# Kernel optimization log

Hardware: AMD Instinct MI355X
Metric: run time of the kernel (lower is better)

Reference implementation:

```python
import jax, jax.numpy as jnp
import numpy as np

B, S, N, C = 128, 512, 64, 1
F = N * C          # flattened feature dim = input_size * n_nodes
H = 512            # hidden_size


def _gru_imputer(x2d, m2d, Wih, Whh, bih, bhh, Wro, bro):
    """Unidirectional 1-step-ahead GRU imputer.
    x2d: [B,S,F] float, m2d: [B,S,F] bool.
    Returns (x_hat [B,S,F], h [B,S,H])."""
    dt = x2d.dtype
    h0 = jnp.zeros((x2d.shape[0], H), dtype=dt)
    xhat0 = h0 @ Wro.T + bro  # readout of initial state (== bro)

    def step(carry, inp):
        h, xhat = carry
        x_t, m_t = inp  # [B,F] float, [B,F] bool
        x_p = jnp.where(m_t, x_t, xhat)
        x_in = jnp.concatenate([x_p, m_t.astype(dt)], axis=-1)  # [B,2F]
        gi = x_in @ Wih.T + bih  # [B,3H]
        gh = h @ Whh.T + bhh     # [B,3H]
        ir, iz, inn = jnp.split(gi, 3, axis=-1)
        hr, hz, hn = jnp.split(gh, 3, axis=-1)
        r = jax.nn.sigmoid(ir + hr)
        z = jax.nn.sigmoid(iz + hz)
        n = jnp.tanh(inn + r * hn)
        h_new = (1.0 - z) * n + z * h
        xhat_new = h_new @ Wro.T + bro
        return (h_new, xhat_new), (h_new, xhat_new)

    xs = (jnp.swapaxes(x2d[:, :-1], 0, 1), jnp.swapaxes(m2d[:, :-1], 0, 1))
    _, (hs, xhats) = jax.lax.scan(step, (h0, xhat0), xs)
    hs = jnp.concatenate([h0[None], hs], axis=0)        # [S,B,H]
    xhats = jnp.concatenate([xhat0[None], xhats], axis=0)  # [S,B,F]
    return jnp.swapaxes(xhats, 0, 1), jnp.swapaxes(hs, 0, 1)


def setup_inputs() -> dict:
    key = jax.random.key(0)
    ks = jax.random.split(key, 16)
    s = 1.0 / np.sqrt(H)
    u = lambda k, shape: jax.random.uniform(k, shape, jnp.float32, -s, s)
    inp = {
        "x": jax.random.normal(ks[0], (B, S, N, C), jnp.float32),
        "mask": jax.random.randint(ks[1], (B, S, N, C), 0, 2).astype(bool),
        # forward-direction RNN params
        "Wih_f": u(ks[2], (3 * H, 2 * F)),
        "Whh_f": u(ks[3], (3 * H, H)),
        "bih_f": u(ks[4], (3 * H,)),
        "bhh_f": u(ks[5], (3 * H,)),
        "Wro_f": u(ks[6], (F, H)),
        "bro_f": u(ks[7], (F,)),
        # backward-direction RNN params
        "Wih_b": u(ks[8], (3 * H, 2 * F)),
        "Whh_b": u(ks[9], (3 * H, H)),
        "bih_b": u(ks[10], (3 * H,)),
        "bhh_b": u(ks[11], (3 * H,)),
        "Wro_b": u(ks[12], (F, H)),
        "bro_b": u(ks[13], (F,)),
        # final bidirectional readout
        "Wout": u(ks[14], (F, 2 * H)),
        "bout": u(ks[15], (F,)),
    }
    return inp


def reference(x, mask, Wih_f, Whh_f, bih_f, bhh_f, Wro_f, bro_f,
              Wih_b, Whh_b, bih_b, bhh_b, Wro_b, bro_b, Wout, bout):
    # rearrange 'b s n c -> b s (n c)'
    x2d = x.reshape(B, S, F)
    m2d = mask.reshape(B, S, F)

    xh_f, h_f = _gru_imputer(x2d, m2d, Wih_f, Whh_f, bih_f, bhh_f, Wro_f, bro_f)
    xh_b, h_b = _gru_imputer(x2d[:, ::-1], m2d[:, ::-1],
                             Wih_b, Whh_b, bih_b, bhh_b, Wro_b, bro_b)
    xh_b = xh_b[:, ::-1]
    h_b = h_b[:, ::-1]

    h = jnp.concatenate([h_f, h_b], axis=-1)  # [B,S,2H]; dropout p=0 -> identity
    x_hat = (h @ Wout.T + bout).reshape(B, S, N, C)
    return (x_hat, xh_f.reshape(B, S, N, C), xh_b.reshape(B, S, N, C))
```

## Files before the change

### kernel.cpp

```cpp
#include <hip/hip_runtime.h>

#define Bx 128
#define Sx 512
#define Fx 64
#define Hx 512
#define Xx 128

#define PARTB_OFF 0ull
#define H_OFF     ((size_t)Bx * Sx * Fx)
#define XH_OFF    (H_OFF + (size_t)2 * 2 * Bx * Hx)
#define BAR_OFF   (XH_OFF + (size_t)2 * Bx * Fx)
#define FLAG_OFF  (BAR_OFF + 4096)

#define LDSW_WHH   0
#define LDSW_XIN   26112
#define LDSW_WRO   (LDSW_XIN + 32 * 160)
#define LDSW_WOUT  (LDSW_WRO + 2 * 544)
#define LDSW_TOTAL (LDSW_WOUT + 2 * 544 + 16)

struct BParams {
  const float* x; const void* mask;
  const float* Wih_f; const float* Whh_f; const float* bih_f; const float* bhh_f;
  const float* Wro_f; const float* bro_f;
  const float* Wih_b; const float* Whh_b; const float* bih_b; const float* bhh_b;
  const float* Wro_b; const float* bro_b;
  const float* Wout; const float* bout;
  float* out; float* ws;
};

__global__ void detect_kernel(const unsigned int* mask, float* ws) {
  int* bars = (int*)(ws + BAR_OFF);
  int* flag = (int*)(ws + FLAG_OFF);
  int t = threadIdx.x;
  for (int i = t; i < 4096; i += blockDim.x) bars[i] = 0;
  if (t == 0) *flag = 0;
  __syncthreads();
  unsigned int v = 0;
  for (int i = t; i < 4096; i += blockDim.x) v |= mask[i] & 0xFFFFFF00u;
  if (v) atomicOr(flag, 1);
}

__global__ void combine_kernel(float* out, const float* partb, const float* bout) {
  int i = blockIdx.x * blockDim.x + threadIdx.x;
  out[i] = out[i] + partb[i] + bout[i & 63];
}

__device__ __forceinline__ float sel8(const float* a, int idx) {
  float v = a[0];
#pragma unroll
  for (int i = 1; i < 8; ++i) v = (idx == i) ? a[i] : v;
  return v;
}

__device__ __forceinline__ void st_sys(float* p, float v) {
  __hip_atomic_store(p, v, __ATOMIC_RELAXED, __HIP_MEMORY_SCOPE_SYSTEM);
}
__device__ __forceinline__ void st_sys_i(int* p, int v) {
  __hip_atomic_store(p, v, __ATOMIC_RELAXED, __HIP_MEMORY_SCOPE_SYSTEM);
}

__device__ __forceinline__ void gbar(int* slots, int hs, int nbar) {
  __syncthreads();
  if (threadIdx.x < 64) {
    if (threadIdx.x == 0) st_sys_i(slots + hs * 16, nbar);
    const int* myslot = slots + (threadIdx.x & 31) * 16;
    for (;;) {
      int v = __hip_atomic_load(myslot, __ATOMIC_RELAXED, __HIP_MEMORY_SCOPE_AGENT);
      if (__all(v >= nbar)) break;
      __builtin_amdgcn_s_sleep(1);
    }
    asm volatile("buffer_inv\n\ts_waitcnt vmcnt(0)" ::: "memory");
  }
  __syncthreads();
}

#define GH_STEP(C, JOFF) {                                                   \
  const float* hr = hrd + (size_t)(j0 + jj + (JOFF)) * Bx + bA;              \
  float4 ha  = *(const float4*)(hr);                                         \
  float4 hbv = *(const float4*)(hr + 4);                                     \
  float s0 = w0.C, s1 = w1.C, s2 = w2.C;                                     \
  acc0[0]=fmaf(s0,ha.x,acc0[0]);  acc0[1]=fmaf(s0,ha.y,acc0[1]);             \
  acc0[2]=fmaf(s0,ha.z,acc0[2]);  acc0[3]=fmaf(s0,ha.w,acc0[3]);             \
  acc0[4]=fmaf(s0,hbv.x,acc0[4]); acc0[5]=fmaf(s0,hbv.y,acc0[5]);            \
  acc0[6]=fmaf(s0,hbv.z,acc0[6]); acc0[7]=fmaf(s0,hbv.w,acc0[7]);            \
  acc1[0]=fmaf(s1,ha.x,acc1[0]);  acc1[1]=fmaf(s1,ha.y,acc1[1]);             \
  acc1[2]=fmaf(s1,ha.z,acc1[2]);  acc1[3]=fmaf(s1,ha.w,acc1[3]);             \
  acc1[4]=fmaf(s1,hbv.x,acc1[4]); acc1[5]=fmaf(s1,hbv.y,acc1[5]);            \
  acc1[6]=fmaf(s1,hbv.z,acc1[6]); acc1[7]=fmaf(s1,hbv.w,acc1[7]);            \
  acc3[0]=fmaf(s2,ha.x,acc3[0]);  acc3[1]=fmaf(s2,ha.y,acc3[1]);             \
  acc3[2]=fmaf(s2,ha.z,acc3[2]);  acc3[3]=fmaf(s2,ha.w,acc3[3]);             \
  acc3[4]=fmaf(s2,hbv.x,acc3[4]); acc3[5]=fmaf(s2,hbv.y,acc3[5]);            \
  acc3[6]=fmaf(s2,hbv.z,acc3[6]); acc3[7]=fmaf(s2,hbv.w,acc3[7]); }

__global__ void __launch_bounds__(512, 2)
birnn_main(BParams p) {
  extern __shared__ float lds[];

  const int w   = blockIdx.x;
  const int g   = w & 7;
  const int dir = g >> 2;
  const int bg  = g & 3;
  const int hs  = w >> 3;
  const int b0  = bg * 32;
  const int u0  = hs * 16;
  const int f0  = hs * 2;
  const int tid = threadIdx.x;

  const float* Wih = dir ? p.Wih_b : p.Wih_f;
  const float* Whh = dir ? p.Whh_b : p.Whh_f;
  const float* bih = dir ? p.bih_b : p.bih_f;
  const float* bhh = dir ? p.bhh_b : p.bhh_f;
  const float* Wro = dir ? p.Wro_b : p.Wro_f;
  const float* bro = dir ? p.bro_b : p.bro_f;

  float* hbuf  = p.ws + H_OFF;
  float* xhb   = p.ws + XH_OFF;
  int*   slots = (int*)(p.ws + BAR_OFF) + g * 512;
  const int u8f = *(const int*)(p.ws + FLAG_OFF);
  const unsigned char* m8  = (const unsigned char*)p.mask;
  const int*           m32 = (const int*)p.mask;

  float* pout   = dir ? (p.ws + PARTB_OFF) : p.out;
  float* out_xh = p.out + (size_t)(1 + dir) * Bx * Sx * Fx;

  for (int idx = tid; idx < 3 * 16 * 512; idx += 512) {
    int g3 = idx >> 13; int rem = idx & 8191;
    int u = rem >> 9;   int j = rem & 511;
    lds[LDSW_WHH + ((g3 * 16 + u) * 8 + (j >> 6)) * 68 + (j & 63)] =
        Whh[(size_t)(g3 * 512 + u0 + u) * Hx + j];
  }
  for (int idx = tid; idx < 2 * 512; idx += 512) {
    int f = idx >> 9, j = idx & 511;
    lds[LDSW_WRO  + f * 544 + (j >> 6) * 68 + (j & 63)] = Wro[(size_t)(f0 + f) * Hx + j];
    lds[LDSW_WOUT + f * 544 + (j >> 6) * 68 + (j & 63)] =
        p.Wout[(size_t)(f0 + f) * (2 * Hx) + dir * Hx + j];
  }

  if (hs == 0) {
    for (int idx = tid; idx < 32 * 512; idx += 512) {
      int u = idx >> 5, bo = idx & 31;
      st_sys(&hbuf[((size_t)(dir * 2 + 0) * Hx + u) * Bx + b0 + bo], 0.f);
    }
  }
  if (tid < 64) {
    int b = b0 + (tid >> 1), f = f0 + (tid & 1);
    float br = bro[f];
    st_sys(&xhb[((size_t)dir * Fx + f) * Bx + b], br);
    int T0 = dir ? (Sx - 1) : 0;
    st_sys(&out_xh[((size_t)b * Sx + T0) * Fx + f], br);
    st_sys(&pout  [((size_t)b * Sx + T0) * Fx + f], 0.f);
  }

  const int jq   = tid & 7;
  const int ulo  = (tid >> 3) & 7;
  const int wv   = tid >> 6;
  const int bsub = wv & 3;
  const int uhi  = wv >> 2;
  const int u    = uhi * 8 + ulo;
  const int bA   = b0 + bsub * 8;
  const int ru   = u0 + u;
  const int j0   = jq * 64;
  const int blo  = (tid >> 3) & 7;
  const int bB   = b0 + (wv & 3) * 8 + blo;
  const int fB   = wv >> 2;

  float4 wih0[4], wih1[4], wih2[4];
#pragma unroll
  for (int q = 0; q < 4; ++q) {
    wih0[q] = *(const float4*)(Wih + (size_t)(0 * 512 + ru) * Xx + jq * 16 + q * 4);
    wih1[q] = *(const float4*)(Wih + (size_t)(1 * 512 + ru) * Xx + jq * 16 + q * 4);
    wih2[q] = *(const float4*)(Wih + (size_t)(2 * 512 + ru) * Xx + jq * 16 + q * 4);
  }
  const float bs_r = bih[ru] + bhh[ru];
  const float bs_z = bih[512 + ru] + bhh[512 + ru];
  const float bs_i = bih[1024 + ru];
  const float bs_h = bhh[1024 + ru];

  const float* w0p = lds + LDSW_WHH + ((0 * 16 + u) * 8 + jq) * 68;
  const float* w1p = lds + LDSW_WHH + ((1 * 16 + u) * 8 + jq) * 68;
  const float* w2p = lds + LDSW_WHH + ((2 * 16 + u) * 8 + jq) * 68;

  float hprev_own = 0.f;

  int nbar = 1;
  gbar(slots, hs, nbar);

  for (int k = 1; k < Sx; ++k) {
    const int pp = k & 1, pr = pp ^ 1;
    const int t_in = dir ? (Sx - k) : (k - 1);

    {
      int bl = tid >> 4, sub = tid & 15;
      int b = b0 + bl;
      float* xr = lds + LDSW_XIN + bl * 160 + (sub >> 1) * 20 + (sub & 1) * 8;
      float v[8];
      if (sub < 8) {
        size_t base = ((size_t)b * Sx + t_in) * Fx + sub * 8;
        float4 xa = *(const float4*)(p.x + base);
        float4 xb = *(const float4*)(p.x + base + 4);
        const float* xhp = xhb + ((size_t)dir * Fx + sub * 8) * Bx + b;
        float h0 = xhp[0 * Bx], h1 = xhp[1 * Bx], h2 = xhp[2 * Bx], h3 = xhp[3 * Bx];
        float h4 = xhp[4 * Bx], h5 = xhp[5 * Bx], h6 = xhp[6 * Bx], h7 = xhp[7 * Bx];
        int mi[8];
        if (u8f) {
          unsigned long long mm = *(const unsigned long long*)(m8 + base);
#pragma unroll
          for (int j = 0; j < 8; ++j) mi[j] = (int)((mm >> (8 * j)) & 0xFF);
        } else {
          int4 ma = *(const int4*)(m32 + base);
          int4 mb = *(const int4*)(m32 + base + 4);
          mi[0] = ma.x; mi[1] = ma.y; mi[2] = ma.z; mi[3] = ma.w;
          mi[4] = mb.x; mi[5] = mb.y; mi[6] = mb.z; mi[7] = mb.w;
        }
        v[0] = mi[0] ? xa.x : h0;  v[1] = mi[1] ? xa.y : h1;
        v[2] = mi[2] ? xa.z : h2;  v[3] = mi[3] ? xa.w : h3;
        v[4] = mi[4] ? xb.x : h4;  v[5] = mi[5] ? xb.y : h5;
        v[6] = mi[6] ? xb.z : h6;  v[7] = mi[7] ? xb.w : h7;
      } else {
        size_t base = ((size_t)b * Sx + t_in) * Fx + (sub - 8) * 8;
        if (u8f) {
          unsigned long long mm = *(const unsigned long long*)(m8 + base);
#pragma unroll
          for (int j = 0; j < 8; ++j) v[j] = (float)((mm >> (8 * j)) & 0xFF);
        } else {
          int4 ma = *(const int4*)(m32 + base);
          int4 mb = *(const int4*)(m32 + base + 4);
          v[0] = (float)ma.x; v[1] = (float)ma.y; v[2] = (float)ma.z; v[3] = (float)ma.w;
          v[4] = (float)mb.x; v[5] = (float)mb.y; v[6] = (float)mb.z; v[7] = (float)mb.w;
        }
      }
      *(float4*)(xr)     = make_float4(v[0], v[1], v[2], v[3]);
      *(float4*)(xr + 4) = make_float4(v[4], v[5], v[6], v[7]);
    }
    __syncthreads();

    float acc0[8], acc1[8], acc2[8], acc3[8];
#pragma unroll
    for (int i = 0; i < 8; ++i) { acc0[i] = 0.f; acc1[i] = 0.f; acc2[i] = 0.f; acc3[i] = 0.f; }

    {
      const float* hrd = hbuf + (size_t)(dir * 2 + pr) * Hx * Bx;
#pragma unroll 2
      for (int jj = 0; jj < 64; jj += 4) {
        float4 w0 = *(const float4*)(w0p + jj);
        float4 w1 = *(const float4*)(w1p + jj);
        float4 w2 = *(const float4*)(w2p + jj);
        GH_STEP(x, 0)
        GH_STEP(y, 1)
        GH_STEP(z, 2)
        GH_STEP(w, 3)
      }
    }
    {
      const float* xinb = lds + LDSW_XIN;
#pragma unroll
      for (int q = 0; q < 4; ++q) {
        float4 w0 = wih0[q], w1 = wih1[q], w2 = wih2[q];
        int off = jq * 20 + q * 4;
#pragma unroll
        for (int bb = 0; bb < 8; ++bb) {
          float4 xv = *(const float4*)(xinb + (bsub * 8 + bb) * 160 + off);
          acc0[bb] = fmaf(w0.x, xv.x, acc0[bb]); acc0[bb] = fmaf(w0.y, xv.y, acc0[bb]);
          acc0[bb] = fmaf(w0.z, xv.z, acc0[bb]); acc0[bb] = fmaf(w0.w, xv.w, acc0[bb]);
          acc1[bb] = fmaf(w1.x, xv.x, acc1[bb]); acc1[bb] = fmaf(w1.y, xv.y, acc1[bb]);
          acc1[bb] = fmaf(w1.z, xv.z, acc1[bb]); acc1[bb] = fmaf(w1.w, xv.w, acc1[bb]);
          acc2[bb] = fmaf(w2.x, xv.x, acc2[bb]); acc2[bb] = fmaf(w2.y, xv.y, acc2[bb]);
          acc2[bb] = fmaf(w2.z, xv.z, acc2[bb]); acc2[bb] = fmaf(w2.w, xv.w, acc2[bb]);
        }
      }
    }
#pragma unroll
    for (int m = 1; m <= 4; m <<= 1) {
#pragma unroll
      for (int bb = 0; bb < 8; ++bb) {
        acc0[bb] += __shfl_xor(acc0[bb], m);
        acc1[bb] += __shfl_xor(acc1[bb], m);
        acc2[bb] += __shfl_xor(acc2[bb], m);
        acc3[bb] += __shfl_xor(acc3[bb], m);
      }
    }
    {
      int b = bA + jq;
      float sr  = sel8(acc0, jq);
      float sz  = sel8(acc1, jq);
      float sgi = sel8(acc2, jq);
      float sgh = sel8(acc3, jq);
      float r = 1.f / (1.f + __expf(-(sr + bs_r)));
      float z = 1.f / (1.f + __expf(-(sz + bs_z)));
      float n = tanhf(sgi + bs_i + r * (sgh + bs_h));
      float hn = (1.f - z) * n + z * hprev_own;
      hprev_own = hn;
      st_sys(&hbuf[((size_t)(dir * 2 + pp) * Hx + ru) * Bx + b], hn);
    }
    ++nbar;
    gbar(slots, hs, nbar);

    {
      const float* hnw  = hbuf + (size_t)(dir * 2 + pp) * Hx * Bx;
      const float* wroL = lds + LDSW_WRO  + fB * 544 + jq * 68;
      const float* wouL = lds + LDSW_WOUT + fB * 544 + jq * 68;
      const float* hcol = hnw + (size_t)j0 * Bx + bB;
      float ax = 0.f, ap = 0.f;
#pragma unroll 4
      for (int jj = 0; jj < 64; jj += 4) {
        float4 wx = *(const float4*)(wroL + jj);
        float4 wp = *(const float4*)(wouL + jj);
        float h0 = hcol[(size_t)(jj + 0) * Bx];
        float h1 = hcol[(size_t)(jj + 1) * Bx];
        float h2 = hcol[(size_t)(jj + 2) * Bx];
        float h3 = hcol[(size_t)(jj + 3) * Bx];
        ax = fmaf(wx.x, h0, ax); ap = fmaf(wp.x, h0, ap);
        ax = fmaf(wx.y, h1, ax); ap = fmaf(wp.y, h1, ap);
        ax = fmaf(wx.z, h2, ax); ap = fmaf(wp.z, h2, ap);
        ax = fmaf(wx.w, h3, ax); ap = fmaf(wp.w, h3, ap);
      }
#pragma unroll
      for (int m = 1; m <= 4; m <<= 1) {
        ax += __shfl_xor(ax, m);
        ap += __shfl_xor(ap, m);
      }
      const int T = dir ? (Sx - 1 - k) : k;
      const int f = f0 + fB;
      if (jq == 0) {
        float v = ax + bro[f];
        st_sys(&xhb[((size_t)dir * Fx + f) * Bx + bB], v);
        st_sys(&out_xh[((size_t)bB * Sx + T) * Fx + f], v);
      } else if (jq == 1) {
        st_sys(&pout[((size_t)bB * Sx + T) * Fx + f], ap);
      }
    }
    ++nbar;
    gbar(slots, hs, nbar);
  }
}

extern "C" void kernel_launch(void* const* d_in, const int* in_sizes, int n_in,
                              void* d_out, int out_size, void* d_ws, size_t ws_size,
                              hipStream_t stream) {
  (void)in_sizes; (void)n_in; (void)out_size; (void)ws_size;
  float* ws = (float*)d_ws;

  detect_kernel<<<1, 512, 0, stream>>>((const unsigned int*)d_in[1], ws);

  BParams p;
  p.x     = (const float*)d_in[0];  p.mask = d_in[1];
  p.Wih_f = (const float*)d_in[2];  p.Whh_f = (const float*)d_in[3];
  p.bih_f = (const float*)d_in[4];  p.bhh_f = (const float*)d_in[5];
  p.Wro_f = (const float*)d_in[6];  p.bro_f = (const float*)d_in[7];
  p.Wih_b = (const float*)d_in[8];  p.Whh_b = (const float*)d_in[9];
  p.bih_b = (const float*)d_in[10]; p.bhh_b = (const float*)d_in[11];
  p.Wro_b = (const float*)d_in[12]; p.bro_b = (const float*)d_in[13];
  p.Wout  = (const float*)d_in[14]; p.bout  = (const float*)d_in[15];
  p.out   = (float*)d_out;
  p.ws    = ws;

  hipFuncSetAttribute(reinterpret_cast<const void*>(birnn_main),
                      hipFuncAttributeMaxDynamicSharedMemorySize,
                      (int)(LDSW_TOTAL * sizeof(float)));
  void* args[] = { (void*)&p };
  hipLaunchCooperativeKernel(reinterpret_cast<void*>(birnn_main),
                             dim3(256), dim3(512), args,
                             (unsigned)(LDSW_TOTAL * sizeof(float)), stream);

  combine_kernel<<<dim3(Bx * Sx * Fx / 256), dim3(256), 0, stream>>>(
      (float*)d_out, ws + PARTB_OFF, (const float*)d_in[15]);
}
```

Before: 22.06 ms.

## Remove per-step second grid barrier via atomic-accumulated readout and deferred output projection

Each CTA now computes the partial readout x_hat from its own 16 hidden units and atomically adds it into a 4-deep rotating global buffer that is pre-seeded with the bias. This removes the second grid-wide barrier per timestep. The Wout partial projection is deferred to the next step, where it runs from the previous hidden state, and the final step is handled after the loop. The change trades one global barrier per step for many atomicAdds and extra rotating buffers, and relies on the buffer-rotation ordering being correct.

```diff
diff --git a/kernel.cpp b/kernel.cpp
--- a/kernel.cpp
+++ b/kernel.cpp
@@ -8,15 +8,17 @@
 
 #define PARTB_OFF 0ull
 #define H_OFF     ((size_t)Bx * Sx * Fx)
-#define XH_OFF    (H_OFF + (size_t)2 * 2 * Bx * Hx)
-#define BAR_OFF   (XH_OFF + (size_t)2 * Bx * Fx)
+#define XHB_OFF   (H_OFF + (size_t)2 * 2 * Hx * Bx)
+#define BAR_OFF   (XHB_OFF + (size_t)4 * 2 * Bx * Fx)
 #define FLAG_OFF  (BAR_OFF + 4096)
 
 #define LDSW_WHH   0
 #define LDSW_XIN   26112
 #define LDSW_WRO   (LDSW_XIN + 32 * 160)
 #define LDSW_WOUT  (LDSW_WRO + 2 * 544)
-#define LDSW_TOTAL (LDSW_WOUT + 2 * 544 + 16)
+#define LDSW_WROS  (LDSW_WOUT + 2 * 544)
+#define LDSW_HX    (LDSW_WROS + 1088)
+#define LDSW_TOTAL (LDSW_HX + 512 + 16)
 
 struct BParams {
   const float* x; const void* mask;
@@ -114,7 +116,7 @@
   const float* bro = dir ? p.bro_b : p.bro_f;
 
   float* hbuf  = p.ws + H_OFF;
-  float* xhb   = p.ws + XH_OFF;
+  float* xhb4  = p.ws + XHB_OFF;
   int*   slots = (int*)(p.ws + BAR_OFF) + g * 512;
   const int u8f = *(const int*)(p.ws + FLAG_OFF);
   const unsigned char* m8  = (const unsigned char*)p.mask;
@@ -135,6 +137,10 @@
     lds[LDSW_WOUT + f * 544 + (j >> 6) * 68 + (j & 63)] =
         p.Wout[(size_t)(f0 + f) * (2 * Hx) + dir * Hx + j];
   }
+  for (int idx = tid; idx < 64 * 16; idx += 512) {
+    int f = idx >> 4, u = idx & 15;
+    lds[LDSW_WROS + f * 17 + u] = Wro[(size_t)f * Hx + u0 + u];
+  }
 
   if (hs == 0) {
     for (int idx = tid; idx < 32 * 512; idx += 512) {
@@ -142,13 +148,12 @@
       st_sys(&hbuf[((size_t)(dir * 2 + 0) * Hx + u) * Bx + b0 + bo], 0.f);
     }
   }
+  float bro_own = 0.f;
   if (tid < 64) {
-    int b = b0 + (tid >> 1), f = f0 + (tid & 1);
-    float br = bro[f];
-    st_sys(&xhb[((size_t)dir * Fx + f) * Bx + b], br);
-    int T0 = dir ? (Sx - 1) : 0;
-    st_sys(&out_xh[((size_t)b * Sx + T0) * Fx + f], br);
-    st_sys(&pout  [((size_t)b * Sx + T0) * Fx + f], 0.f);
+    bro_own = bro[tid];
+#pragma unroll
+    for (int q = 0; q < 4; ++q)
+      st_sys(&xhb4[(((size_t)q * 2 + dir) * Bx + (b0 + hs)) * Fx + tid], bro_own);
   }
 
   const int jq   = tid & 7;
@@ -163,6 +168,8 @@
   const int blo  = (tid >> 3) & 7;
   const int bB   = b0 + (wv & 3) * 8 + blo;
   const int fB   = wv >> 2;
+  const int pf   = tid & 63;
+  const int pbq  = tid >> 6;
 
   float4 wih0[4], wih1[4], wih2[4];
 #pragma unroll
@@ -188,6 +195,9 @@
   for (int k = 1; k < Sx; ++k) {
     const int pp = k & 1, pr = pp ^ 1;
     const int t_in = dir ? (Sx - k) : (k - 1);
+    const int rdq = (k - 1) & 3;
+    const int adq = k & 3;
+    const int inq = (k + 2) & 3;
 
     {
       int bl = tid >> 4, sub = tid & 15;
@@ -198,9 +208,9 @@
         size_t base = ((size_t)b * Sx + t_in) * Fx + sub * 8;
         float4 xa = *(const float4*)(p.x + base);
         float4 xb = *(const float4*)(p.x + base + 4);
-        const float* xhp = xhb + ((size_t)dir * Fx + sub * 8) * Bx + b;
-        float h0 = xhp[0 * Bx], h1 = xhp[1 * Bx], h2 = xhp[2 * Bx], h3 = xhp[3 * Bx];
-        float h4 = xhp[4 * Bx], h5 = xhp[5 * Bx], h6 = xhp[6 * Bx], h7 = xhp[7 * Bx];
+        const float* xhp = xhb4 + (((size_t)rdq * 2 + dir) * Bx + b) * Fx + sub * 8;
+        float4 ha  = *(const float4*)(xhp);
+        float4 hb4 = *(const float4*)(xhp + 4);
         int mi[8];
         if (u8f) {
           unsigned long long mm = *(const unsigned long long*)(m8 + base);
@@ -212,10 +222,10 @@
           mi[0] = ma.x; mi[1] = ma.y; mi[2] = ma.z; mi[3] = ma.w;
           mi[4] = mb.x; mi[5] = mb.y; mi[6] = mb.z; mi[7] = mb.w;
         }
-        v[0] = mi[0] ? xa.x : h0;  v[1] = mi[1] ? xa.y : h1;
-        v[2] = mi[2] ? xa.z : h2;  v[3] = mi[3] ? xa.w : h3;
-        v[4] = mi[4] ? xb.x : h4;  v[5] = mi[5] ? xb.y : h5;
-        v[6] = mi[6] ? xb.z : h6;  v[7] = mi[7] ? xb.w : h7;
+        v[0] = mi[0] ? xa.x : ha.x;  v[1] = mi[1] ? xa.y : ha.y;
+        v[2] = mi[2] ? xa.z : ha.z;  v[3] = mi[3] ? xa.w : ha.w;
+        v[4] = mi[4] ? xb.x : hb4.x; v[5] = mi[5] ? xb.y : hb4.y;
+        v[6] = mi[6] ? xb.z : hb4.z; v[7] = mi[7] ? xb.w : hb4.w;
       } else {
         size_t base = ((size_t)b * Sx + t_in) * Fx + (sub - 8) * 8;
         if (u8f) {
@@ -231,6 +241,30 @@
       }
       *(float4*)(xr)     = make_float4(v[0], v[1], v[2], v[3]);
       *(float4*)(xr + 4) = make_float4(v[4], v[5], v[6], v[7]);
+    }
+    if (tid < 64) {
+      float v = xhb4[(((size_t)rdq * 2 + dir) * Bx + (b0 + hs)) * Fx + tid];
+      st_sys(&out_xh[((size_t)(b0 + hs) * Sx + t_in) * Fx + tid], v);
+    }
+    {
+      const float* hnw  = hbuf + (size_t)(dir * 2 + pr) * Hx * Bx;
+      const float* wouL = lds + LDSW_WOUT + fB * 544 + jq * 68;
+      const float* hcol = hnw + (size_t)j0 * Bx + bB;
+      float ap = 0.f;
+#pragma unroll 4
+      for (int jj = 0; jj < 64; jj += 4) {
+        float4 wp = *(const float4*)(wouL + jj);
+        float h0 = hcol[(size_t)(jj + 0) * Bx];
+        float h1 = hcol[(size_t)(jj + 1) * Bx];
+        float h2 = hcol[(size_t)(jj + 2) * Bx];
+        float h3 = hcol[(size_t)(jj + 3) * Bx];
+        ap = fmaf(wp.x, h0, ap); ap = fmaf(wp.y, h1, ap);
+        ap = fmaf(wp.z, h2, ap); ap = fmaf(wp.w, h3, ap);
+      }
+#pragma unroll
+      for (int m = 1; m <= 4; m <<= 1) ap += __shfl_xor(ap, m);
+      if (jq == 0)
+        st_sys(&pout[((size_t)bB * Sx + t_in) * Fx + f0 + fB], ap);
     }
     __syncthreads();
 
@@ -291,46 +325,61 @@
       float hn = (1.f - z) * n + z * hprev_own;
       hprev_own = hn;
       st_sys(&hbuf[((size_t)(dir * 2 + pp) * Hx + ru) * Bx + b], hn);
-    }
+      lds[LDSW_HX + (bsub * 8 + jq) * 16 + u] = hn;
+    }
+    __syncthreads();
+
+    {
+      const float* wros = lds + LDSW_WROS + pf * 17;
+      float* xq = xhb4 + (((size_t)adq * 2 + dir) * Bx + b0) * Fx;
+#pragma unroll
+      for (int i = 0; i < 4; ++i) {
+        int bl = pbq * 4 + i;
+        const float* hx = lds + LDSW_HX + bl * 16;
+        float s = 0.f;
+#pragma unroll
+        for (int uu = 0; uu < 16; ++uu) s = fmaf(wros[uu], hx[uu], s);
+        atomicAdd(xq + (size_t)bl * Fx + pf, s);
+      }
+    }
+    if (tid < 64)
+      st_sys(&xhb4[(((size_t)inq * 2 + dir) * Bx + (b0 + hs)) * Fx + tid], bro_own);
+
     ++nbar;
     gbar(slots, hs, nbar);
-
-    {
-      const float* hnw  = hbuf + (size_t)(dir * 2 + pp) * Hx * Bx;
-      const float* wroL = lds + LDSW_WRO  + fB * 544 + jq * 68;
-      const float* wouL = lds + LDSW_WOUT + fB * 544 + jq * 68;
-      const float* hcol = hnw + (size_t)j0 * Bx + bB;
-      float ax = 0.f, ap = 0.f;
+  }
+
+  {
+    const int ppE = (Sx - 1) & 1;
+    const int tE  = dir ? 0 : (Sx - 1);
+    const float* hnw  = hbuf + (size_t)(dir * 2 + ppE) * Hx * Bx;
+    const float* wroL = lds + LDSW_WRO  + fB * 544 + jq * 68;
+    const float* wouL = lds + LDSW_WOUT + fB * 544 + jq * 68;
+    const float* hcol = hnw + (size_t)j0 * Bx + bB;
+    float ax = 0.f, ap = 0.f;
 #pragma unroll 4
-      for (int jj = 0; jj < 64; jj += 4) {
-        float4 wx = *(const float4*)(wroL + jj);
-        float4 wp = *(const float4*)(wouL + jj);
-        float h0 = hcol[(size_t)(jj + 0) * Bx];
-        float h1 = hcol[(size_t)(jj + 1) * Bx];
-        float h2 = hcol[(size_t)(jj + 2) * Bx];
-        float h3 = hcol[(size_t)(jj + 3) * Bx];
-        ax = fmaf(wx.x, h0, ax); ap = fmaf(wp.x, h0, ap);
-        ax = fmaf(wx.y, h1, ax); ap = fmaf(wp.y, h1, ap);
-        ax = fmaf(wx.z, h2, ax); ap = fmaf(wp.z, h2, ap);
-        ax = fmaf(wx.w, h3, ax); ap = fmaf(wp.w, h3, ap);
-      }
-#pragma unroll
-      for (int m = 1; m <= 4; m <<= 1) {
-        ax += __shfl_xor(ax, m);
-        ap += __shfl_xor(ap, m);
-      }
-      const int T = dir ? (Sx - 1 - k) : k;
-      const int f = f0 + fB;
-      if (jq == 0) {
-        float v = ax + bro[f];
-        st_sys(&xhb[((size_t)dir * Fx + f) * Bx + bB], v);
-        st_sys(&out_xh[((size_t)bB * Sx + T) * Fx + f], v);
-      } else if (jq == 1) {
-        st_sys(&pout[((size_t)bB * Sx + T) * Fx + f], ap);
-      }
-    }
-    ++nbar;
-    gbar(slots, hs, nbar);
+    for (int jj = 0; jj < 64; jj += 4) {
+      float4 wx = *(const float4*)(wroL + jj);
+      float4 wp = *(const float4*)(wouL + jj);
+      float h0 = hcol[(size_t)(jj + 0) * Bx];
+      float h1 = hcol[(size_t)(jj + 1) * Bx];
+      float h2 = hcol[(size_t)(jj + 2) * Bx];
+      float h3 = hcol[(size_t)(jj + 3) * Bx];
+      ax = fmaf(wx.x, h0, ax); ap = fmaf(wp.x, h0, ap);
+      ax = fmaf(wx.y, h1, ax); ap = fmaf(wp.y, h1, ap);
+      ax = fmaf(wx.z, h2, ax); ap = fmaf(wp.z, h2, ap);
+      ax = fmaf(wx.w, h3, ax); ap = fmaf(wp.w, h3, ap);
+    }
+#pragma unroll
+    for (int m = 1; m <= 4; m <<= 1) {
+      ax += __shfl_xor(ax, m);
+      ap += __shfl_xor(ap, m);
+    }
+    const int f = f0 + fB;
+    if (jq == 0)
+      st_sys(&out_xh[((size_t)bB * Sx + tE) * Fx + f], ax + bro[f]);
+    else if (jq == 1)
+      st_sys(&pout[((size_t)bB * Sx + tE) * Fx + f], ap);
   }
 }
 
```

Result: faster. 21.13 ms (-4.2%).
